# Performance work log

Measured on AMD Instinct MI355X. Metric: run time of the kernel, lower is better.

## Reference

```python
import jax, jax.numpy as jnp
import numpy as np

B, S, E, H, L = 16, 1024, 512, 8, 4
D = E // H  # head_dim = 64


def setup_inputs() -> dict:
    key = jax.random.key(0)
    ks = jax.random.split(key, 16)
    std = 0.02
    inp = {
        "q": jax.random.normal(ks[0], (B, S, E), jnp.float32),
        "k": jax.random.normal(ks[1], (B, S, E), jnp.float32),
        "v": jax.random.normal(ks[2], (B, S, E), jnp.float32),
        # standard Linear params (torch convention: W is (out, in))
        "Wq": jax.random.normal(ks[3], (E, E), jnp.float32) * std,
        "bq": jnp.zeros((E,), jnp.float32),
        "Wk": jax.random.normal(ks[4], (E, E), jnp.float32) * std,
        "bk": jnp.zeros((E,), jnp.float32),
        # WFLinear: shared weight elementwise-multiplied by per-language factor
        "Wv_share": jax.random.normal(ks[5], (E, E), jnp.float32) * std,
        "Wv_spec": 1.0 + jax.random.normal(ks[6], (L, E, E), jnp.float32) * std,
        "bv_share": jnp.zeros((E,), jnp.float32),
        "bv_spec": jax.random.normal(ks[7], (L, E), jnp.float32) * std,
        "Wo_share": jax.random.normal(ks[8], (E, E), jnp.float32) * std,
        "Wo_spec": 1.0 + jax.random.normal(ks[9], (L, E, E), jnp.float32) * std,
        "bo_share": jnp.zeros((E,), jnp.float32),
        "bo_spec": jax.random.normal(ks[10], (L, E), jnp.float32) * std,
        "mask": jax.random.randint(ks[11], (B, S), 0, 2, jnp.int32),
        "languageID": 1,
    }
    return inp


def reference(q, k, v, Wq, bq, Wk, bk, Wv_share, Wv_spec, bv_share, bv_spec,
              Wo_share, Wo_spec, bo_share, bo_spec, mask, languageID):
    scaling = D ** (-0.5)
    # projections (torch Linear: x @ W.T + b)
    Q = (q @ Wq.T + bq).reshape(B, S, H, D).transpose(0, 2, 1, 3) * scaling
    K = (k @ Wk.T + bk).reshape(B, S, H, D).transpose(0, 2, 1, 3)
    Wv = Wv_share * Wv_spec[languageID]
    bv = bv_share + bv_spec[languageID]
    V = (v @ Wv.T + bv).reshape(B, S, H, D).transpose(0, 2, 1, 3)
    # NOTE: faithful to original — Q already scaled by d_k^-0.5, and
    # AttentionWF divides by sqrt(d_k) AGAIN (effective scale 1/d_k).
    alpha = jnp.einsum("bhqd,bhkd->bhqk", Q, K) / np.float32(np.sqrt(D))
    m = (mask == 0)[:, None, None, :]  # (B,1,1,S) over key axis
    alpha = jnp.where(m, jnp.float32(-1e9), alpha)
    alpha = jax.nn.softmax(alpha, axis=-1)
    # dropout p=0.0 -> identity
    ctx = jnp.einsum("bhqk,bhkd->bhqd", alpha, V)  # (B,H,S,D)
    concat = ctx.transpose(0, 2, 1, 3).reshape(B, S, E)
    Wo = Wo_share * Wo_spec[languageID]
    bo = bo_share + bo_spec[languageID]
    return concat @ Wo.T + bo
```

## Files before the change

kernel.cpp:

```cpp
#include <hip/hip_runtime.h>

#define B_ 16
#define S_ 1024
#define E_ 512
#define H_ 8
#define D_ 64
#define L_ 4
#define M_ (B_*S_)

typedef unsigned short u16;
typedef __attribute__((ext_vector_type(8))) short bf16x8;
typedef __attribute__((ext_vector_type(4))) float f32x4;
typedef __attribute__((ext_vector_type(4))) unsigned uint4v;

__device__ __forceinline__ u16 f2bf(float x) {
  unsigned u = __float_as_uint(x);
  unsigned r = (u + 0x7fffu + ((u >> 16) & 1u)) >> 16;
  return (u16)r;
}
__device__ __forceinline__ ushort4 f2bf4(float4 f) {
  ushort4 u;
  u.x = f2bf(f.x); u.y = f2bf(f.y); u.z = f2bf(f.z); u.w = f2bf(f.w);
  return u;
}
__device__ __forceinline__ unsigned cvt_pk_bf16(float lo, float hi) {
  unsigned r;
  asm("v_cvt_pk_bf16_f32 %0, %1, %2" : "=v"(r) : "v"(lo), "v"(hi));
  return r;
}

typedef __attribute__((address_space(1))) const void gconst_void;
typedef __attribute__((address_space(3))) void lds_void;
__device__ __forceinline__ void gl_lds16(const void* g, void* l) {
  __builtin_amdgcn_global_load_lds((gconst_void*)g, (lds_void*)l, 16, 0, 0);
}

__global__ __launch_bounds__(256) void prep_w(
    const float* __restrict__ Wq, const float* __restrict__ Wk,
    const float* __restrict__ Wv_sh, const float* __restrict__ Wv_sp,
    const float* __restrict__ Wo_sh, const float* __restrict__ Wo_sp,
    const float* __restrict__ bv_sh, const float* __restrict__ bv_sp,
    const float* __restrict__ bo_sh, const float* __restrict__ bo_sp,
    const int* __restrict__ langp,
    u16* __restrict__ Wq_b, u16* __restrict__ Wk_b,
    u16* __restrict__ Wv_b, u16* __restrict__ Wo_b,
    float* __restrict__ bv_f, float* __restrict__ bo_f) {
  int lang = langp[0];
  int i = blockIdx.x * 256 + threadIdx.x;
  size_t wofs = (size_t)lang * (E_*E_/4) + i;
  ((ushort4*)Wq_b)[i] = f2bf4(((const float4*)Wq)[i]);
  ((ushort4*)Wk_b)[i] = f2bf4(((const float4*)Wk)[i]);
  float4 vs = ((const float4*)Wv_sh)[i], vp = ((const float4*)Wv_sp)[wofs];
  float4 os = ((const float4*)Wo_sh)[i], op = ((const float4*)Wo_sp)[wofs];
  float4 vv = {vs.x*vp.x, vs.y*vp.y, vs.z*vp.z, vs.w*vp.w};
  float4 oo = {os.x*op.x, os.y*op.y, os.z*op.z, os.w*op.w};
  ((ushort4*)Wv_b)[i] = f2bf4(vv);
  ((ushort4*)Wo_b)[i] = f2bf4(oo);
  if (i < E_/4) {
    float4 b1 = ((const float4*)bv_sh)[i], b2 = ((const float4*)(bv_sp + (size_t)lang*E_))[i];
    float4 b3 = ((const float4*)bo_sh)[i], b4 = ((const float4*)(bo_sp + (size_t)lang*E_))[i];
    float4 r1 = {b1.x+b2.x, b1.y+b2.y, b1.z+b2.z, b1.w+b2.w};
    float4 r2 = {b3.x+b4.x, b3.y+b4.y, b3.z+b4.z, b3.w+b4.w};
    ((float4*)bv_f)[i] = r1;
    ((float4*)bo_f)[i] = r2;
  }
}

__global__ __launch_bounds__(256) void gemm_qkv(
    const float* __restrict__ q, const float* __restrict__ k, const float* __restrict__ v,
    const u16* __restrict__ Wq_b, const u16* __restrict__ Wk_b, const u16* __restrict__ Wv_b,
    const float* __restrict__ bq, const float* __restrict__ bk, const float* __restrict__ bv,
    u16* __restrict__ Qb, u16* __restrict__ Kb, u16* __restrict__ Vb) {
  __shared__ __align__(16) float sAf[128*32];
  __shared__ __align__(16) u16 sB[128*32];
  const int z = blockIdx.y;
  const float* A    = (z == 0) ? q : (z == 1) ? k : v;
  const u16*   Bw   = (z == 0) ? Wq_b : (z == 1) ? Wk_b : Wv_b;
  const float* bias = (z == 0) ? bq : (z == 1) ? bk : bv;
  u16*         out  = (z == 0) ? Qb : (z == 1) ? Kb : Vb;
  const int t = threadIdx.x;
  const int hw = blockIdx.x;
  const int wk = (hw & 7) * 64 + (hw >> 3);
  const int m0 = (wk >> 2) * 128, n0 = (wk & 3) * 128;
  const int lane = t & 63, wid = t >> 6;
  const int m16 = lane & 15, qq = lane >> 4;
  const int wrow = (wid >> 1) * 64, wcol = (wid & 1) * 64;
  f32x4 acc[4][4] = {};
  const int ca0 = wid*4;
  const float* ap[4];
  float* sap[4];
#pragma unroll
  for (int i = 0; i < 4; ++i) {
    int ca = ca0 + i;
    ap[i]  = A + (size_t)(m0 + ca*8 + (lane >> 3)) * E_ + (lane & 7) * 4;
    sap[i] = &sAf[ca * 256];
  }
  const int cb0 = wid*2, cb1 = wid*2 + 1;
  const u16* bp0 = Bw + (size_t)(n0 + cb0*16 + (lane >> 2)) * E_ + (lane & 3) * 8;
  const u16* bp1 = Bw + (size_t)(n0 + cb1*16 + (lane >> 2)) * E_ + (lane & 3) * 8;
  u16* sbp0 = &sB[cb0 * 512];
  u16* sbp1 = &sB[cb1 * 512];
  for (int k0 = 0; k0 < E_; k0 += 32) {
#pragma unroll
    for (int i = 0; i < 4; ++i) gl_lds16(ap[i], sap[i]);
    gl_lds16(bp0, sbp0);
    gl_lds16(bp1, sbp1);
    __syncthreads();
    bf16x8 af[4], bfm[4];
#pragma unroll
    for (int mt = 0; mt < 4; ++mt) {
      const float* ar = &sAf[(wrow + mt*16 + m16) * 32 + qq*8];
      f32x4 a0 = *(const f32x4*)ar;
      f32x4 a1 = *(const f32x4*)(ar + 4);
      union { uint4v u; bf16x8 h; } cv;
      cv.u = (uint4v){ cvt_pk_bf16(a0[0], a0[1]), cvt_pk_bf16(a0[2], a0[3]),
                       cvt_pk_bf16(a1[0], a1[1]), cvt_pk_bf16(a1[2], a1[3]) };
      af[mt] = cv.h;
    }
#pragma unroll
    for (int nt = 0; nt < 4; ++nt)
      bfm[nt] = *(const bf16x8*)&sB[(wcol + nt*16 + m16) * 32 + qq*8];
#pragma unroll
    for (int mt = 0; mt < 4; ++mt)
#pragma unroll
      for (int nt = 0; nt < 4; ++nt)
        acc[mt][nt] = __builtin_amdgcn_mfma_f32_16x16x32_bf16(af[mt], bfm[nt], acc[mt][nt], 0, 0, 0);
    __syncthreads();
#pragma unroll
    for (int i = 0; i < 4; ++i) ap[i] += 32;
    bp0 += 32; bp1 += 32;
  }
  float bvv[4];
#pragma unroll
  for (int nt = 0; nt < 4; ++nt) bvv[nt] = bias[n0 + wcol + nt*16 + m16];
#pragma unroll
  for (int mt = 0; mt < 4; ++mt) {
    int gm = m0 + wrow + mt*16 + qq*4;
#pragma unroll
    for (int nt = 0; nt < 4; ++nt) {
      int gn = n0 + wcol + nt*16 + m16;
#pragma unroll
      for (int r = 0; r < 4; ++r)
        out[(size_t)(gm + r) * E_ + gn] = f2bf(acc[mt][nt][r] + bvv[nt]);
    }
  }
}

__global__ __launch_bounds__(256) void gemm_lds(
    const u16* __restrict__ A, const u16* __restrict__ Bw,
    const float* __restrict__ bias, float* __restrict__ out) {
  __shared__ __align__(16) u16 sA[128*32];
  __shared__ __align__(16) u16 sB[128*32];
  const int t = threadIdx.x;
  const int hw = blockIdx.x;
  const int wk = (hw & 7) * 64 + (hw >> 3);
  const int m0 = (wk >> 2) * 128, n0 = (wk & 3) * 128;
  const int lane = t & 63, wid = t >> 6;
  const int m16 = lane & 15, qq = lane >> 4;
  const int wrow = (wid >> 1) * 64, wcol = (wid & 1) * 64;
  f32x4 acc[4][4] = {};
  const int c0 = 2*wid, c1 = 2*wid + 1;
  const int colk = (lane & 3) * 8;
  const int r0 = c0*16 + (lane >> 2), r1 = c1*16 + (lane >> 2);
  const u16* a0 = A  + (size_t)(m0 + r0) * E_ + colk;
  const u16* a1 = A  + (size_t)(m0 + r1) * E_ + colk;
  const u16* b0 = Bw + (size_t)(n0 + r0) * E_ + colk;
  const u16* b1 = Bw + (size_t)(n0 + r1) * E_ + colk;
  u16* sa0 = &sA[c0*512]; u16* sa1 = &sA[c1*512];
  u16* sb0 = &sB[c0*512]; u16* sb1 = &sB[c1*512];
  for (int k0 = 0; k0 < E_; k0 += 32) {
    gl_lds16(a0, sa0);
    gl_lds16(a1, sa1);
    gl_lds16(b0, sb0);
    gl_lds16(b1, sb1);
    __syncthreads();
    bf16x8 af[4], bfm[4];
#pragma unroll
    for (int mt = 0; mt < 4; ++mt)
      af[mt] = *(const bf16x8*)&sA[(wrow + mt*16 + m16) * 32 + qq*8];
#pragma unroll
    for (int nt = 0; nt < 4; ++nt)
      bfm[nt] = *(const bf16x8*)&sB[(wcol + nt*16 + m16) * 32 + qq*8];
#pragma unroll
    for (int mt = 0; mt < 4; ++mt)
#pragma unroll
      for (int nt = 0; nt < 4; ++nt)
        acc[mt][nt] = __builtin_amdgcn_mfma_f32_16x16x32_bf16(af[mt], bfm[nt], acc[mt][nt], 0, 0, 0);
    __syncthreads();
    a0 += 32; a1 += 32; b0 += 32; b1 += 32;
  }
  float bv[4];
#pragma unroll
  for (int nt = 0; nt < 4; ++nt) bv[nt] = bias[n0 + wcol + nt*16 + m16];
#pragma unroll
  for (int mt = 0; mt < 4; ++mt) {
    int gm = m0 + wrow + mt*16 + qq*4;
#pragma unroll
    for (int nt = 0; nt < 4; ++nt) {
      int gn = n0 + wcol + nt*16 + m16;
#pragma unroll
      for (int r = 0; r < 4; ++r)
        out[(size_t)(gm + r) * E_ + gn] = acc[mt][nt][r] + bv[nt];
    }
  }
}

#define TS_ 72
__global__ __launch_bounds__(256) void transpose_v(const u16* __restrict__ Vb,
                                                   u16* __restrict__ Vt) {
  __shared__ __align__(16) u16 sT[64*TS_];
  const int t = threadIdx.x;
  const int bh = blockIdx.y, b = bh >> 3, h = bh & 7;
  const int s0 = blockIdx.x * 64;
  const int row = t >> 2, c0 = (t & 3) * 16;
  const u16* src = Vb + (size_t)(b*S_ + s0 + row) * E_ + h*D_ + c0;
  *(uint4*)&sT[row*TS_ + c0]     = *(const uint4*)src;
  *(uint4*)&sT[row*TS_ + c0 + 8] = *(const uint4*)(src + 8);
  __syncthreads();
  const int d = t >> 2, sc = (t & 3) * 16;
  unsigned w[8];
#pragma unroll
  for (int i = 0; i < 8; ++i) {
    unsigned lo = sT[(sc + 2*i    ) * TS_ + d];
    unsigned hi = sT[(sc + 2*i + 1) * TS_ + d];
    w[i] = lo | (hi << 16);
  }
  u16* dst = Vt + ((size_t)(b*H_ + h) * D_ + d) * S_ + s0 + sc;
  uint4 p0 = {w[0], w[1], w[2], w[3]}, p1 = {w[4], w[5], w[6], w[7]};
  *(uint4*)dst = p0;
  *(uint4*)(dst + 8) = p1;
}

#define KST 72
__global__ __launch_bounds__(256) void attn_mfma(
    const u16* __restrict__ Qb, const u16* __restrict__ Kb, const u16* __restrict__ Vt,
    const int* __restrict__ mask, u16* __restrict__ ctxb) {
  __shared__ __align__(16) u16 sK[64*KST];
  __shared__ __align__(16) u16 sV[64*KST];
  __shared__ __align__(16) u16 sP[64*KST];
  __shared__ __align__(16) float sMask[64];
  __shared__ __align__(16) float sL[64];
  const int t = threadIdx.x;
  const int lane = t & 63, w = t >> 6;
  const int m16 = lane & 15, quad = lane >> 4;
  const int hw = blockIdx.x;
  const int wk = (hw & 7) * 256 + (hw >> 3);
  const int bh = wk >> 4, b = bh >> 3, h = bh & 7;
  const int qblk = (wk & 15) * 64;
  const int q0 = qblk + w * 16;
  bf16x8 qf0, qf1;
  {
    const u16* qp = Qb + (size_t)(b*S_ + q0 + m16) * E_ + h*D_ + quad*8;
    qf0 = *(const bf16x8*)qp;
    qf1 = *(const bf16x8*)(qp + 32);
  }
  f32x4 oacc[4] = {};
  float lpart = 0.f;
  const int srow = t >> 2, sc0 = (t & 3) * 16;
  const u16* kp = Kb + (size_t)(b*S_ + srow) * E_ + h*D_ + sc0;
  const u16* vp = Vt + ((size_t)(b*H_ + h) * D_ + srow) * S_ + sc0;
  uint4 rk0 = *(const uint4*)kp, rk1 = *(const uint4*)(kp + 8);
  uint4 rv0 = *(const uint4*)vp, rv1 = *(const uint4*)(vp + 8);
  float rmsk = 0.f;
  if (t < 64) rmsk = (mask[b*S_ + t] == 0) ? -1e9f : 0.f;
  const float CS = 0.015625f * 1.44269504f;
  for (int kt = 0; kt < S_; kt += 64) {
    *(uint4*)&sK[srow*KST + sc0]     = rk0;
    *(uint4*)&sK[srow*KST + sc0 + 8] = rk1;
    *(uint4*)&sV[srow*KST + sc0]     = rv0;
    *(uint4*)&sV[srow*KST + sc0 + 8] = rv1;
    if (t < 64) sMask[t] = rmsk;
    __syncthreads();
    if (kt + 64 < S_) {
      kp += (size_t)64 * E_; vp += 64;
      rk0 = *(const uint4*)kp; rk1 = *(const uint4*)(kp + 8);
      rv0 = *(const uint4*)vp; rv1 = *(const uint4*)(vp + 8);
      if (t < 64) rmsk = (mask[b*S_ + kt + 64 + t] == 0) ? -1e9f : 0.f;
    }
    f32x4 sacc[4] = {};
#pragma unroll
    for (int ct = 0; ct < 4; ++ct) {
      bf16x8 kf0 = *(const bf16x8*)&sK[(ct*16 + m16)*KST + quad*8];
      bf16x8 kf1 = *(const bf16x8*)&sK[(ct*16 + m16)*KST + 32 + quad*8];
      sacc[ct] = __builtin_amdgcn_mfma_f32_16x16x32_bf16(kf0, qf0, sacc[ct], 0, 0, 0);
      sacc[ct] = __builtin_amdgcn_mfma_f32_16x16x32_bf16(kf1, qf1, sacc[ct], 0, 0, 0);
    }
#pragma unroll
    for (int ct = 0; ct < 4; ++ct) {
      f32x4 msk = *(const f32x4*)&sMask[ct*16 + quad*4];
      float p0 = exp2f(fmaf(sacc[ct][0], CS, msk[0]));
      float p1 = exp2f(fmaf(sacc[ct][1], CS, msk[1]));
      float p2 = exp2f(fmaf(sacc[ct][2], CS, msk[2]));
      float p3 = exp2f(fmaf(sacc[ct][3], CS, msk[3]));
      lpart += (p0 + p1) + (p2 + p3);
      uint2 pq = { cvt_pk_bf16(p0, p1), cvt_pk_bf16(p2, p3) };
      *(uint2*)&sP[(w*16 + m16)*KST + ct*16 + quad*4] = pq;
    }
    bf16x8 pf0 = *(const bf16x8*)&sP[(w*16 + m16)*KST + quad*8];
    bf16x8 pf1 = *(const bf16x8*)&sP[(w*16 + m16)*KST + 32 + quad*8];
#pragma unroll
    for (int dt = 0; dt < 4; ++dt) {
      bf16x8 vf0 = *(const bf16x8*)&sV[(dt*16 + m16)*KST + quad*8];
      bf16x8 vf1 = *(const bf16x8*)&sV[(dt*16 + m16)*KST + 32 + quad*8];
      oacc[dt] = __builtin_amdgcn_mfma_f32_16x16x32_bf16(pf0, vf0, oacc[dt], 0, 0, 0);
      oacc[dt] = __builtin_amdgcn_mfma_f32_16x16x32_bf16(pf1, vf1, oacc[dt], 0, 0, 0);
    }
    __syncthreads();
  }
  lpart += __shfl_xor(lpart, 16);
  lpart += __shfl_xor(lpart, 32);
  if (quad == 0) sL[w*16 + m16] = lpart;
  float inv[4];
#pragma unroll
  for (int r = 0; r < 4; ++r) inv[r] = 1.0f / sL[w*16 + quad*4 + r];
#pragma unroll
  for (int dt = 0; dt < 4; ++dt)
#pragma unroll
    for (int r = 0; r < 4; ++r)
      sP[(w*16 + quad*4 + r)*KST + dt*16 + m16] = f2bf(oacc[dt][r] * inv[r]);
  __syncthreads();
  const int orow = t >> 2, oc0 = (t & 3) * 16;
  uint4 o0 = *(uint4*)&sP[orow*KST + oc0];
  uint4 o1 = *(uint4*)&sP[orow*KST + oc0 + 8];
  u16* dst = ctxb + (size_t)(b*S_ + qblk + orow) * E_ + h*D_ + oc0;
  *(uint4*)dst = o0;
  *(uint4*)(dst + 8) = o1;
}

extern "C" void kernel_launch(void* const* d_in, const int* in_sizes, int n_in,
                              void* d_out, int out_size, void* d_ws, size_t ws_size,
                              hipStream_t stream) {
  const float* q     = (const float*)d_in[0];
  const float* k     = (const float*)d_in[1];
  const float* v     = (const float*)d_in[2];
  const float* Wq    = (const float*)d_in[3];
  const float* bq    = (const float*)d_in[4];
  const float* Wk    = (const float*)d_in[5];
  const float* bk    = (const float*)d_in[6];
  const float* Wv_sh = (const float*)d_in[7];
  const float* Wv_sp = (const float*)d_in[8];
  const float* bv_sh = (const float*)d_in[9];
  const float* bv_sp = (const float*)d_in[10];
  const float* Wo_sh = (const float*)d_in[11];
  const float* Wo_sp = (const float*)d_in[12];
  const float* bo_sh = (const float*)d_in[13];
  const float* bo_sp = (const float*)d_in[14];
  const int*   mask  = (const int*)d_in[15];
  const int*   lang  = (const int*)d_in[16];

  char* ws = (char*)d_ws;
  size_t off = 0;
  auto alloc = [&](size_t bytes) -> char* {
    char* p = ws + off;
    off += (bytes + 255) & ~(size_t)255;
    return p;
  };
  u16* Qb   = (u16*)alloc((size_t)M_ * E_ * 2);
  u16* Kb   = (u16*)alloc((size_t)M_ * E_ * 2);
  u16* Vb   = (u16*)alloc((size_t)M_ * E_ * 2);
  u16* Vt   = (u16*)alloc((size_t)M_ * E_ * 2);
  u16* ctxb = (u16*)alloc((size_t)M_ * E_ * 2);
  u16* Wq_b = (u16*)alloc((size_t)E_ * E_ * 2);
  u16* Wk_b = (u16*)alloc((size_t)E_ * E_ * 2);
  u16* Wv_b = (u16*)alloc((size_t)E_ * E_ * 2);
  u16* Wo_b = (u16*)alloc((size_t)E_ * E_ * 2);
  float* bv_f = (float*)alloc(E_ * 4);
  float* bo_f = (float*)alloc(E_ * 4);

  prep_w<<<E_*E_/1024, 256, 0, stream>>>(Wq, Wk, Wv_sh, Wv_sp, Wo_sh, Wo_sp,
                                         bv_sh, bv_sp, bo_sh, bo_sp, lang,
                                         Wq_b, Wk_b, Wv_b, Wo_b, bv_f, bo_f);

  dim3 qkvgrid(512, 3);
  gemm_qkv<<<qkvgrid, 256, 0, stream>>>(q, k, v, Wq_b, Wk_b, Wv_b,
                                        bq, bk, bv_f, Qb, Kb, Vb);

  dim3 tgrid(S_/64, B_*H_);
  transpose_v<<<tgrid, 256, 0, stream>>>(Vb, Vt);

  attn_mfma<<<2048, 256, 0, stream>>>(Qb, Kb, Vt, mask, ctxb);

  gemm_lds<<<512, 256, 0, stream>>>(ctxb, Wo_b, bo_f, (float*)d_out);
}
```

Before: 310.1 us.

## Double-buffer GEMM LDS tiles and write V transposed from QKV epilogue

Both projection GEMMs now use two LDS buffers, issuing the next k-tile's global-to-LDS loads before computing on the current tile, with one waitcnt+barrier per iteration instead of two syncthreads. The QKV GEMM epilogue writes the V projection directly in transposed (b,h,d,s) layout, which removes the separate transpose kernel and the intermediate Vb buffer. This doubles LDS use per block, which may lower occupancy, and the transposed stores are narrow 8-byte writes strided across rows.

```diff
diff --git a/kernel.cpp b/kernel.cpp
--- a/kernel.cpp
+++ b/kernel.cpp
@@ -33,6 +33,10 @@
 typedef __attribute__((address_space(3))) void lds_void;
 __device__ __forceinline__ void gl_lds16(const void* g, void* l) {
   __builtin_amdgcn_global_load_lds((gconst_void*)g, (lds_void*)l, 16, 0, 0);
+}
+__device__ __forceinline__ void fence_vm0_barrier() {
+  asm volatile("s_waitcnt vmcnt(0)" ::: "memory");
+  __builtin_amdgcn_s_barrier();
 }
 
 __global__ __launch_bounds__(256) void prep_w(
@@ -66,18 +70,18 @@
   }
 }
 
+#define QBUF 4096
 __global__ __launch_bounds__(256) void gemm_qkv(
     const float* __restrict__ q, const float* __restrict__ k, const float* __restrict__ v,
     const u16* __restrict__ Wq_b, const u16* __restrict__ Wk_b, const u16* __restrict__ Wv_b,
     const float* __restrict__ bq, const float* __restrict__ bk, const float* __restrict__ bv,
-    u16* __restrict__ Qb, u16* __restrict__ Kb, u16* __restrict__ Vb) {
-  __shared__ __align__(16) float sAf[128*32];
-  __shared__ __align__(16) u16 sB[128*32];
+    u16* __restrict__ Qb, u16* __restrict__ Kb, u16* __restrict__ Vt) {
+  __shared__ __align__(16) float sAfD[2*QBUF];
+  __shared__ __align__(16) u16   sBD[2*QBUF];
   const int z = blockIdx.y;
   const float* A    = (z == 0) ? q : (z == 1) ? k : v;
   const u16*   Bw   = (z == 0) ? Wq_b : (z == 1) ? Wk_b : Wv_b;
   const float* bias = (z == 0) ? bq : (z == 1) ? bk : bv;
-  u16*         out  = (z == 0) ? Qb : (z == 1) ? Kb : Vb;
   const int t = threadIdx.x;
   const int hw = blockIdx.x;
   const int wk = (hw & 7) * 64 + (hw >> 3);
@@ -88,28 +92,40 @@
   f32x4 acc[4][4] = {};
   const int ca0 = wid*4;
   const float* ap[4];
-  float* sap[4];
-#pragma unroll
-  for (int i = 0; i < 4; ++i) {
-    int ca = ca0 + i;
-    ap[i]  = A + (size_t)(m0 + ca*8 + (lane >> 3)) * E_ + (lane & 7) * 4;
-    sap[i] = &sAf[ca * 256];
-  }
+#pragma unroll
+  for (int i = 0; i < 4; ++i)
+    ap[i] = A + (size_t)(m0 + (ca0+i)*8 + (lane >> 3)) * E_ + (lane & 7) * 4;
   const int cb0 = wid*2, cb1 = wid*2 + 1;
   const u16* bp0 = Bw + (size_t)(n0 + cb0*16 + (lane >> 2)) * E_ + (lane & 3) * 8;
   const u16* bp1 = Bw + (size_t)(n0 + cb1*16 + (lane >> 2)) * E_ + (lane & 3) * 8;
-  u16* sbp0 = &sB[cb0 * 512];
-  u16* sbp1 = &sB[cb1 * 512];
-  for (int k0 = 0; k0 < E_; k0 += 32) {
-#pragma unroll
-    for (int i = 0; i < 4; ++i) gl_lds16(ap[i], sap[i]);
-    gl_lds16(bp0, sbp0);
-    gl_lds16(bp1, sbp1);
-    __syncthreads();
+  {
+#pragma unroll
+    for (int i = 0; i < 4; ++i) gl_lds16(ap[i], &sAfD[(ca0+i)*256]);
+    gl_lds16(bp0, &sBD[cb0*512]);
+    gl_lds16(bp1, &sBD[cb1*512]);
+#pragma unroll
+    for (int i = 0; i < 4; ++i) ap[i] += 32;
+    bp0 += 32; bp1 += 32;
+  }
+  fence_vm0_barrier();
+  for (int kt = 0; kt < 16; ++kt) {
+    if (kt < 15) {
+      float* sa = &sAfD[((kt+1)&1)*QBUF];
+      u16*   sb = &sBD[((kt+1)&1)*QBUF];
+#pragma unroll
+      for (int i = 0; i < 4; ++i) gl_lds16(ap[i], sa + (ca0+i)*256);
+      gl_lds16(bp0, sb + cb0*512);
+      gl_lds16(bp1, sb + cb1*512);
+#pragma unroll
+      for (int i = 0; i < 4; ++i) ap[i] += 32;
+      bp0 += 32; bp1 += 32;
+    }
+    const float* saf = &sAfD[(kt&1)*QBUF];
+    const u16*   sbb = &sBD[(kt&1)*QBUF];
     bf16x8 af[4], bfm[4];
 #pragma unroll
     for (int mt = 0; mt < 4; ++mt) {
-      const float* ar = &sAf[(wrow + mt*16 + m16) * 32 + qq*8];
+      const float* ar = saf + (wrow + mt*16 + m16) * 32 + qq*8;
       f32x4 a0 = *(const f32x4*)ar;
       f32x4 a1 = *(const f32x4*)(ar + 4);
       union { uint4v u; bf16x8 h; } cv;
@@ -119,29 +135,42 @@
     }
 #pragma unroll
     for (int nt = 0; nt < 4; ++nt)
-      bfm[nt] = *(const bf16x8*)&sB[(wcol + nt*16 + m16) * 32 + qq*8];
+      bfm[nt] = *(const bf16x8*)(sbb + (wcol + nt*16 + m16) * 32 + qq*8);
 #pragma unroll
     for (int mt = 0; mt < 4; ++mt)
 #pragma unroll
       for (int nt = 0; nt < 4; ++nt)
         acc[mt][nt] = __builtin_amdgcn_mfma_f32_16x16x32_bf16(af[mt], bfm[nt], acc[mt][nt], 0, 0, 0);
-    __syncthreads();
-#pragma unroll
-    for (int i = 0; i < 4; ++i) ap[i] += 32;
-    bp0 += 32; bp1 += 32;
+    if (kt < 15) fence_vm0_barrier();
   }
   float bvv[4];
 #pragma unroll
   for (int nt = 0; nt < 4; ++nt) bvv[nt] = bias[n0 + wcol + nt*16 + m16];
-#pragma unroll
-  for (int mt = 0; mt < 4; ++mt) {
-    int gm = m0 + wrow + mt*16 + qq*4;
-#pragma unroll
-    for (int nt = 0; nt < 4; ++nt) {
-      int gn = n0 + wcol + nt*16 + m16;
-#pragma unroll
-      for (int r = 0; r < 4; ++r)
-        out[(size_t)(gm + r) * E_ + gn] = f2bf(acc[mt][nt][r] + bvv[nt]);
+  if (z < 2) {
+    u16* out = (z == 0) ? Qb : Kb;
+#pragma unroll
+    for (int mt = 0; mt < 4; ++mt) {
+      int gm = m0 + wrow + mt*16 + qq*4;
+#pragma unroll
+      for (int nt = 0; nt < 4; ++nt) {
+        int gn = n0 + wcol + nt*16 + m16;
+#pragma unroll
+        for (int r = 0; r < 4; ++r)
+          out[(size_t)(gm + r) * E_ + gn] = f2bf(acc[mt][nt][r] + bvv[nt]);
+      }
+    }
+  } else {
+#pragma unroll
+    for (int mt = 0; mt < 4; ++mt) {
+      int tok0 = m0 + wrow + mt*16 + qq*4;
+      int bb = tok0 >> 10, s0 = tok0 & 1023;
+#pragma unroll
+      for (int nt = 0; nt < 4; ++nt) {
+        int dim = n0 + wcol + nt*16 + m16;
+        uint2 wv = { cvt_pk_bf16(acc[mt][nt][0] + bvv[nt], acc[mt][nt][1] + bvv[nt]),
+                     cvt_pk_bf16(acc[mt][nt][2] + bvv[nt], acc[mt][nt][3] + bvv[nt]) };
+        *(uint2*)(Vt + ((size_t)(bb*E_ + dim))*S_ + s0) = wv;
+      }
     }
   }
 }
@@ -149,8 +178,8 @@
 __global__ __launch_bounds__(256) void gemm_lds(
     const u16* __restrict__ A, const u16* __restrict__ Bw,
     const float* __restrict__ bias, float* __restrict__ out) {
-  __shared__ __align__(16) u16 sA[128*32];
-  __shared__ __align__(16) u16 sB[128*32];
+  __shared__ __align__(16) u16 sAD[2*QBUF];
+  __shared__ __align__(16) u16 sBD[2*QBUF];
   const int t = threadIdx.x;
   const int hw = blockIdx.x;
   const int wk = (hw & 7) * 64 + (hw >> 3);
@@ -166,28 +195,37 @@
   const u16* a1 = A  + (size_t)(m0 + r1) * E_ + colk;
   const u16* b0 = Bw + (size_t)(n0 + r0) * E_ + colk;
   const u16* b1 = Bw + (size_t)(n0 + r1) * E_ + colk;
-  u16* sa0 = &sA[c0*512]; u16* sa1 = &sA[c1*512];
-  u16* sb0 = &sB[c0*512]; u16* sb1 = &sB[c1*512];
-  for (int k0 = 0; k0 < E_; k0 += 32) {
-    gl_lds16(a0, sa0);
-    gl_lds16(a1, sa1);
-    gl_lds16(b0, sb0);
-    gl_lds16(b1, sb1);
-    __syncthreads();
+  gl_lds16(a0, &sAD[c0*512]);
+  gl_lds16(a1, &sAD[c1*512]);
+  gl_lds16(b0, &sBD[c0*512]);
+  gl_lds16(b1, &sBD[c1*512]);
+  a0 += 32; a1 += 32; b0 += 32; b1 += 32;
+  fence_vm0_barrier();
+  for (int kt = 0; kt < 16; ++kt) {
+    if (kt < 15) {
+      u16* sa = &sAD[((kt+1)&1)*QBUF];
+      u16* sb = &sBD[((kt+1)&1)*QBUF];
+      gl_lds16(a0, sa + c0*512);
+      gl_lds16(a1, sa + c1*512);
+      gl_lds16(b0, sb + c0*512);
+      gl_lds16(b1, sb + c1*512);
+      a0 += 32; a1 += 32; b0 += 32; b1 += 32;
+    }
+    const u16* sa = &sAD[(kt&1)*QBUF];
+    const u16* sb = &sBD[(kt&1)*QBUF];
     bf16x8 af[4], bfm[4];
 #pragma unroll
     for (int mt = 0; mt < 4; ++mt)
-      af[mt] = *(const bf16x8*)&sA[(wrow + mt*16 + m16) * 32 + qq*8];
+      af[mt] = *(const bf16x8*)(sa + (wrow + mt*16 + m16) * 32 + qq*8);
 #pragma unroll
     for (int nt = 0; nt < 4; ++nt)
-      bfm[nt] = *(const bf16x8*)&sB[(wcol + nt*16 + m16) * 32 + qq*8];
+      bfm[nt] = *(const bf16x8*)(sb + (wcol + nt*16 + m16) * 32 + qq*8);
 #pragma unroll
     for (int mt = 0; mt < 4; ++mt)
 #pragma unroll
       for (int nt = 0; nt < 4; ++nt)
         acc[mt][nt] = __builtin_amdgcn_mfma_f32_16x16x32_bf16(af[mt], bfm[nt], acc[mt][nt], 0, 0, 0);
-    __syncthreads();
-    a0 += 32; a1 += 32; b0 += 32; b1 += 32;
+    if (kt < 15) fence_vm0_barrier();
   }
   float bv[4];
 #pragma unroll
@@ -203,32 +241,6 @@
         out[(size_t)(gm + r) * E_ + gn] = acc[mt][nt][r] + bv[nt];
     }
   }
-}
-
-#define TS_ 72
-__global__ __launch_bounds__(256) void transpose_v(const u16* __restrict__ Vb,
-                                                   u16* __restrict__ Vt) {
-  __shared__ __align__(16) u16 sT[64*TS_];
-  const int t = threadIdx.x;
-  const int bh = blockIdx.y, b = bh >> 3, h = bh & 7;
-  const int s0 = blockIdx.x * 64;
-  const int row = t >> 2, c0 = (t & 3) * 16;
-  const u16* src = Vb + (size_t)(b*S_ + s0 + row) * E_ + h*D_ + c0;
-  *(uint4*)&sT[row*TS_ + c0]     = *(const uint4*)src;
-  *(uint4*)&sT[row*TS_ + c0 + 8] = *(const uint4*)(src + 8);
-  __syncthreads();
-  const int d = t >> 2, sc = (t & 3) * 16;
-  unsigned w[8];
-#pragma unroll
-  for (int i = 0; i < 8; ++i) {
-    unsigned lo = sT[(sc + 2*i    ) * TS_ + d];
-    unsigned hi = sT[(sc + 2*i + 1) * TS_ + d];
-    w[i] = lo | (hi << 16);
-  }
-  u16* dst = Vt + ((size_t)(b*H_ + h) * D_ + d) * S_ + s0 + sc;
-  uint4 p0 = {w[0], w[1], w[2], w[3]}, p1 = {w[4], w[5], w[6], w[7]};
-  *(uint4*)dst = p0;
-  *(uint4*)(dst + 8) = p1;
 }
 
 #define KST 72
@@ -357,7 +369,6 @@
   };
   u16* Qb   = (u16*)alloc((size_t)M_ * E_ * 2);
   u16* Kb   = (u16*)alloc((size_t)M_ * E_ * 2);
-  u16* Vb   = (u16*)alloc((size_t)M_ * E_ * 2);
   u16* Vt   = (u16*)alloc((size_t)M_ * E_ * 2);
   u16* ctxb = (u16*)alloc((size_t)M_ * E_ * 2);
   u16* Wq_b = (u16*)alloc((size_t)E_ * E_ * 2);
@@ -373,10 +384,7 @@
 
   dim3 qkvgrid(512, 3);
   gemm_qkv<<<qkvgrid, 256, 0, stream>>>(q, k, v, Wq_b, Wk_b, Wv_b,
-                                        bq, bk, bv_f, Qb, Kb, Vb);
-
-  dim3 tgrid(S_/64, B_*H_);
-  transpose_v<<<tgrid, 256, 0, stream>>>(Vb, Vt);
+                                        bq, bk, bv_f, Qb, Kb, Vt);
 
   attn_mfma<<<2048, 256, 0, stream>>>(Qb, Kb, Vt, mask, ctxb);
 
```

New measurement: 309.9 us. About the same (-0.1%).
